# Performance work log

Measured on AMD Instinct MI355X. Metric: run time of the kernel, lower is better.

The kernel has to match this reference:

```python
import jax, jax.numpy as jnp
import numpy as np

B, T, C, H = 8, 2048, 1024, 128

def setup_inputs() -> dict:
    key = jax.random.key(0)
    kx, kq, kk, kv = jax.random.split(key, 4)
    x = jax.random.normal(kx, (B, T, C), dtype=jnp.float32)
    Wq = jax.random.normal(kq, (C, H), dtype=jnp.float32) * 0.02
    Wk = jax.random.normal(kk, (C, H), dtype=jnp.float32) * 0.02
    Wv = jax.random.normal(kv, (C, H), dtype=jnp.float32) * 0.02
    return {"x": x, "Wq": Wq, "Wk": Wk, "Wv": Wv}

def reference(x, Wq, Wk, Wv):
    # q,k,v: [B,T,H] via bias-free dense projections
    q = jnp.einsum('btc,ch->bth', x, Wq)
    k = jnp.einsum('btc,ch->bth', x, Wk)
    v = jnp.einsum('btc,ch->bth', x, Wv)
    scale = k.shape[-1] ** (-0.5)
    # scores: [B,T,T]
    wei = jnp.einsum('bth,bsh->bts', q, k) * scale
    Tlen = x.shape[1]
    causal = jnp.tril(jnp.ones((Tlen, Tlen), dtype=bool))  # True = keep
    wei = jnp.where(causal[None, :, :], wei, -jnp.inf)
    wei = jax.nn.softmax(wei, axis=-1)
    return jnp.einsum('bts,bsh->bth', wei, v)
```

## Files before the change

kernel.cpp:

```cpp
#include <hip/hip_runtime.h>

#define B_ 8
#define T_ 2048
#define C_ 1024
#define H_ 128
#define BT_ (B_*T_)

typedef unsigned short u16;
typedef unsigned int u32;
typedef __attribute__((ext_vector_type(4))) float f32x4;
typedef __attribute__((ext_vector_type(8))) __bf16 bf16x8;

__device__ __forceinline__ u16 f2bf(float f) {
  u32 u = __float_as_uint(f);
  u += 0x7fffu + ((u >> 16) & 1u);
  return (u16)(u >> 16);
}

#define GLL16(g, l) __builtin_amdgcn_global_load_lds( \
    (const __attribute__((address_space(1))) void*)(g), \
    (__attribute__((address_space(3))) void*)(l), 16, 0, 0)

__device__ __forceinline__ bf16x8 load_frag(const u16* base, int stride, int row0, int k0, int lane) {
  const u16* p = base + (size_t)(row0 + (lane & 15)) * stride + k0 + ((lane >> 4) << 3);
  return *reinterpret_cast<const bf16x8*>(p);
}

__device__ __forceinline__ bf16x8 cvt8(f32x4 lo, f32x4 hi) {
  union { u16 h[8]; bf16x8 v; } u;
#pragma unroll
  for (int i = 0; i < 4; i++) { u.h[i] = f2bf(lo[i]); u.h[4 + i] = f2bf(hi[i]); }
  return u.v;
}

__global__ void wt_kernel(const float* __restrict__ Wq, const float* __restrict__ Wk,
                          const float* __restrict__ Wv, u16* __restrict__ wt) {
  int mat = blockIdx.y;
  const float* W = (mat == 0) ? Wq : (mat == 1) ? Wk : Wv;
  int i = blockIdx.x * 256 + threadIdx.x;
  int h = i >> 10;
  int c = i & 1023;
  wt[mat * (C_ * H_) + i] = f2bf(W[c * H_ + h]);
}

__global__ __launch_bounds__(256) void qkv_gemm(const float* __restrict__ x, const u16* __restrict__ wt,
                                                u16* __restrict__ q, u16* __restrict__ k2,
                                                u16* __restrict__ vt) {
  __shared__ __align__(16) float As[2][64 * 32];
  __shared__ __align__(16) u16 Bs[2][128 * 32];
  int t = threadIdx.x;
  int lane = t & 63, w = t >> 6;
  int wm = w >> 1, wn = w & 1;
  int quad = lane >> 4, col = lane & 15;
  int m0 = blockIdx.x * 64;
  int mat = blockIdx.y;
  const u16* wmp = wt + (size_t)mat * (C_ * H_);

  int ar0 = t >> 3, ar1 = ar0 + 32;
  const float* ax0 = x + (size_t)(m0 + ar0) * C_ + (((t & 7) ^ (ar0 & 7)) << 2);
  const float* ax1 = x + (size_t)(m0 + ar1) * C_ + (((t & 7) ^ (ar1 & 7)) << 2);
  const u16* bw0 = wmp + (size_t)(t >> 2) * C_ + ((t & 3) << 3);
  const u16* bw1 = bw0 + (size_t)64 * C_;

  GLL16(ax0, &As[0][w * 256]);
  GLL16(ax1, &As[0][w * 256 + 1024]);
  GLL16(bw0, &Bs[0][w * 512]);
  GLL16(bw1, &Bs[0][2048 + w * 512]);

  f32x4 acc[2][4] = {};
  for (int kk = 0; kk < 32; kk++) {
    int cur = kk & 1;
    __syncthreads();
    if (kk + 1 < 32) {
      int nxt = cur ^ 1;
      int kn = (kk + 1) * 32;
      GLL16(ax0 + kn, &As[nxt][w * 256]);
      GLL16(ax1 + kn, &As[nxt][w * 256 + 1024]);
      GLL16(bw0 + kn, &Bs[nxt][w * 512]);
      GLL16(bw1 + kn, &Bs[nxt][2048 + w * 512]);
    }
    const float* Ab = &As[cur][0];
    const u16* Bb = &Bs[cur][0];
    bf16x8 af[2];
#pragma unroll
    for (int mt = 0; mt < 2; mt++) {
      int r = wm * 32 + mt * 16 + col;
      int s0 = (quad * 2) ^ (r & 7);
      int s1 = s0 ^ 1;
      f32x4 lo = *reinterpret_cast<const f32x4*>(Ab + r * 32 + s0 * 4);
      f32x4 hi = *reinterpret_cast<const f32x4*>(Ab + r * 32 + s1 * 4);
      af[mt] = cvt8(lo, hi);
    }
    bf16x8 bfr[4];
#pragma unroll
    for (int nt = 0; nt < 4; nt++) {
      int n = wn * 64 + nt * 16 + col;
      bfr[nt] = *reinterpret_cast<const bf16x8*>(Bb + n * 32 + quad * 8);
    }
#pragma unroll
    for (int mt = 0; mt < 2; mt++)
#pragma unroll
      for (int nt = 0; nt < 4; nt++)
        acc[mt][nt] = __builtin_amdgcn_mfma_f32_16x16x32_bf16(af[mt], bfr[nt], acc[mt][nt], 0, 0, 0);
  }

#pragma unroll
  for (int mt = 0; mt < 2; mt++) {
    int row0 = m0 + wm * 32 + mt * 16 + quad * 4;
#pragma unroll
    for (int nt = 0; nt < 4; nt++) {
      int n = wn * 64 + nt * 16 + col;
      if (mat == 0) {
#pragma unroll
        for (int r = 0; r < 4; r++) q[(size_t)(row0 + r) * H_ + n] = f2bf(acc[mt][nt][r]);
      } else if (mat == 1) {
#pragma unroll
        for (int r = 0; r < 4; r++) k2[(size_t)(row0 + r) * H_ + n] = f2bf(acc[mt][nt][r]);
      } else {
        int bb = row0 >> 11, tt = row0 & 2047;
        ushort4 pk;
        pk.x = f2bf(acc[mt][nt][0]); pk.y = f2bf(acc[mt][nt][1]);
        pk.z = f2bf(acc[mt][nt][2]); pk.w = f2bf(acc[mt][nt][3]);
        *reinterpret_cast<ushort4*>(&vt[((size_t)bb * H_ + n) * T_ + tt]) = pk;
      }
    }
  }
}

__global__ __launch_bounds__(256) void attn_part(const u16* __restrict__ q, const u16* __restrict__ k,
                                                 const u16* __restrict__ vt,
                                                 float* __restrict__ Op, float* __restrict__ lsum) {
  __shared__ __align__(16) u16 Ks[2][32 * 136];
  __shared__ __align__(16) u16 Vs[2][128 * 40];
  __shared__ __align__(16) u16 P[4][2][16 * 40];
  int t = threadIdx.x;
  int lane = t & 63, w = t >> 6;
  int quad = lane >> 4, col = lane & 15;
  int bx = blockIdx.x;
  int qt = 31 - (bx >> 4);
  int s = (bx >> 3) & 1;
  int b = bx & 7;
  const float scale = 0.08838834764831845f;

  int nk = 2 * (qt + 1);
  int n0 = qt + 1;
  int it0 = s ? n0 : 0;
  int it1 = s ? nk : n0;

  int krow0 = t >> 4, ke = (t & 15) * 8;
  int krow1 = krow0 + 16;
  int vrow0 = t >> 2, ve = (t & 3) * 8;
  int vrow1 = vrow0 + 64;

  int qrow0 = b * T_ + qt * 64 + w * 16;
  bf16x8 qf[4];
#pragma unroll
  for (int ks = 0; ks < 4; ks++) qf[ks] = load_frag(q, H_, qrow0, ks * 32, lane);

  f32x4 o[8] = {};
  float l[4] = {0.f, 0.f, 0.f, 0.f};
  int myqrow = qt * 64 + w * 16 + quad * 4;

  {
    const u16* kb = k + (size_t)(b * T_ + it0 * 32) * H_;
    *reinterpret_cast<uint4*>(&Ks[0][krow0 * 136 + ke]) = *reinterpret_cast<const uint4*>(kb + (size_t)krow0 * 128 + ke);
    *reinterpret_cast<uint4*>(&Ks[0][krow1 * 136 + ke]) = *reinterpret_cast<const uint4*>(kb + (size_t)krow1 * 128 + ke);
    const u16* vb = vt + (size_t)b * H_ * T_ + it0 * 32;
    *reinterpret_cast<uint4*>(&Vs[0][vrow0 * 40 + ve]) = *reinterpret_cast<const uint4*>(vb + (size_t)vrow0 * T_ + ve);
    *reinterpret_cast<uint4*>(&Vs[0][vrow1 * 40 + ve]) = *reinterpret_cast<const uint4*>(vb + (size_t)vrow1 * T_ + ve);
  }

  for (int kt = it0; kt < it1; kt++) {
    int cur = (kt - it0) & 1;
    __syncthreads();
    bool more = (kt + 1 < it1);
    uint4 kc0, kc1, vc0, vc1;
    if (more) {
      const u16* kb = k + (size_t)(b * T_ + (kt + 1) * 32) * H_;
      kc0 = *reinterpret_cast<const uint4*>(kb + (size_t)krow0 * 128 + ke);
      kc1 = *reinterpret_cast<const uint4*>(kb + (size_t)krow1 * 128 + ke);
      const u16* vb = vt + (size_t)b * H_ * T_ + (kt + 1) * 32;
      vc0 = *reinterpret_cast<const uint4*>(vb + (size_t)vrow0 * T_ + ve);
      vc1 = *reinterpret_cast<const uint4*>(vb + (size_t)vrow1 * T_ + ve);
    }

    f32x4 s0 = {}, s1 = {};
#pragma unroll
    for (int ks = 0; ks < 4; ks++) {
      bf16x8 kb0 = *reinterpret_cast<const bf16x8*>(&Ks[cur][col * 136 + ks * 32 + quad * 8]);
      bf16x8 kb1 = *reinterpret_cast<const bf16x8*>(&Ks[cur][(col + 16) * 136 + ks * 32 + quad * 8]);
      s0 = __builtin_amdgcn_mfma_f32_16x16x32_bf16(qf[ks], kb0, s0, 0, 0, 0);
      s1 = __builtin_amdgcn_mfma_f32_16x16x32_bf16(qf[ks], kb1, s1, 0, 0, 0);
    }

    float pv[8];
    int kcol0 = kt * 32 + col;
#pragma unroll
    for (int r = 0; r < 4; r++) {
      int qr = myqrow + r;
      float a0 = fminf(s0[r] * scale, 30.f);
      float a1 = fminf(s1[r] * scale, 30.f);
      a0 = (kcol0      > qr) ? -1e30f : a0;
      a1 = (kcol0 + 16 > qr) ? -1e30f : a1;
      float p0 = __expf(a0);
      float p1 = __expf(a1);
      pv[r] = p0; pv[4 + r] = p1;
      l[r] += p0 + p1;
    }

    u16* Pb = &P[w][cur][0];
#pragma unroll
    for (int r = 0; r < 4; r++) {
      Pb[(quad * 4 + r) * 40 + col] = f2bf(pv[r]);
      Pb[(quad * 4 + r) * 40 + col + 16] = f2bf(pv[4 + r]);
    }
    asm volatile("" ::: "memory");
    __builtin_amdgcn_s_waitcnt(0xc07f);
    asm volatile("" ::: "memory");
    bf16x8 pf = *reinterpret_cast<const bf16x8*>(&Pb[col * 40 + (quad << 3)]);

#pragma unroll
    for (int ht = 0; ht < 8; ht++) {
      bf16x8 vf = *reinterpret_cast<const bf16x8*>(&Vs[cur][(ht * 16 + col) * 40 + quad * 8]);
      o[ht] = __builtin_amdgcn_mfma_f32_16x16x32_bf16(pf, vf, o[ht], 0, 0, 0);
    }

    if (more) {
      int nxt = cur ^ 1;
      *reinterpret_cast<uint4*>(&Ks[nxt][krow0 * 136 + ke]) = kc0;
      *reinterpret_cast<uint4*>(&Ks[nxt][krow1 * 136 + ke]) = kc1;
      *reinterpret_cast<uint4*>(&Vs[nxt][vrow0 * 40 + ve]) = vc0;
      *reinterpret_cast<uint4*>(&Vs[nxt][vrow1 * 40 + ve]) = vc1;
    }
  }

#pragma unroll
  for (int r = 0; r < 4; r++) {
    float v = l[r];
    v += __shfl_xor(v, 1);
    v += __shfl_xor(v, 2);
    v += __shfl_xor(v, 4);
    v += __shfl_xor(v, 8);
    l[r] = v;
  }

  int tile = (s * 8 + b) * 32 + qt;
  float* Orow = Op + (size_t)tile * (64 * 128);
  float* lrow = lsum + (size_t)tile * 64;
  int rowin0 = w * 16 + quad * 4;
  if (col == 0) {
#pragma unroll
    for (int r = 0; r < 4; r++) lrow[rowin0 + r] = l[r];
  }
#pragma unroll
  for (int ht = 0; ht < 8; ht++) {
#pragma unroll
    for (int r = 0; r < 4; r++)
      Orow[(size_t)(rowin0 + r) * 128 + ht * 16 + col] = o[ht][r];
  }
}

__global__ __launch_bounds__(256) void attn_comb(const float* __restrict__ Op, const float* __restrict__ lsum,
                                                 float* __restrict__ out) {
  int bx = blockIdx.x;
  int b = bx >> 5, qt = bx & 31;
  int t = threadIdx.x;
  int h = t & 127, half = t >> 7;
  int tile0 = b * 32 + qt;
  int tile1 = tile0 + 256;
#pragma unroll 4
  for (int rr = 0; rr < 32; rr++) {
    int row = half * 32 + rr;
    float l0 = lsum[tile0 * 64 + row];
    float l1 = lsum[tile1 * 64 + row];
    float rl = 1.f / (l0 + l1);
    float v = (Op[(size_t)tile0 * 8192 + row * 128 + h] +
               Op[(size_t)tile1 * 8192 + row * 128 + h]) * rl;
    out[((size_t)(b * T_ + qt * 64 + row)) * H_ + h] = v;
  }
}

extern "C" void kernel_launch(void* const* d_in, const int* in_sizes, int n_in,
                              void* d_out, int out_size, void* d_ws, size_t ws_size,
                              hipStream_t stream) {
  (void)in_sizes; (void)n_in; (void)out_size; (void)ws_size;
  const float* x  = (const float*)d_in[0];
  const float* Wq = (const float*)d_in[1];
  const float* Wk = (const float*)d_in[2];
  const float* Wv = (const float*)d_in[3];
  u16* ws = (u16*)d_ws;
  u16* q  = ws;
  u16* k  = ws + (size_t)BT_ * H_;
  u16* vt = ws + 2 * (size_t)BT_ * H_;
  u16* wt = ws + 3 * (size_t)BT_ * H_;
  float* Op = (float*)(ws + 3 * (size_t)BT_ * H_ + 3 * C_ * H_);
  float* lsum = Op + (size_t)512 * 64 * 128;
  float* out = (float*)d_out;

  wt_kernel<<<dim3(512, 3), 256, 0, stream>>>(Wq, Wk, Wv, wt);
  qkv_gemm<<<dim3(BT_ / 64, 3), 256, 0, stream>>>(x, wt, q, k, vt);
  attn_part<<<dim3(512), 256, 0, stream>>>(q, k, vt, Op, lsum);
  attn_comb<<<dim3(256), 256, 0, stream>>>(Op, lsum, out);
}
```

Baseline: 175.6 us.

## Deepen QKV GEMM pipeline to 4-stage LDS ring with explicit vmcnt waits

Replaces the double-buffered K loop in the QKV projection GEMM with a 4-buffer LDS ring that keeps three stages of global-to-LDS loads in flight. Each iteration waits with an explicit s_waitcnt vmcnt(8) and a raw barrier, then issues the stage three iterations ahead. The aim is to hide more global-load latency. It also swaps the manual round-to-nearest bf16 conversion for native __bf16 casts, which may lower to hardware convert instructions. The ring doubles LDS use and may reduce occupancy. The trailing iterations issue redundant wrapped loads (stage index mod 32). Correctness relies on the hand-written vmcnt count matching the number of outstanding loads.

```diff
diff --git a/kernel.cpp b/kernel.cpp
--- a/kernel.cpp
+++ b/kernel.cpp
@@ -26,11 +26,11 @@
   return *reinterpret_cast<const bf16x8*>(p);
 }
 
-__device__ __forceinline__ bf16x8 cvt8(f32x4 lo, f32x4 hi) {
-  union { u16 h[8]; bf16x8 v; } u;
-#pragma unroll
-  for (int i = 0; i < 4; i++) { u.h[i] = f2bf(lo[i]); u.h[4 + i] = f2bf(hi[i]); }
-  return u.v;
+__device__ __forceinline__ bf16x8 cvt8n(f32x4 lo, f32x4 hi) {
+  bf16x8 r;
+#pragma unroll
+  for (int i = 0; i < 4; i++) { r[i] = (__bf16)lo[i]; r[4 + i] = (__bf16)hi[i]; }
+  return r;
 }
 
 __global__ void wt_kernel(const float* __restrict__ Wq, const float* __restrict__ Wk,
@@ -46,8 +46,8 @@
 __global__ __launch_bounds__(256) void qkv_gemm(const float* __restrict__ x, const u16* __restrict__ wt,
                                                 u16* __restrict__ q, u16* __restrict__ k2,
                                                 u16* __restrict__ vt) {
-  __shared__ __align__(16) float As[2][64 * 32];
-  __shared__ __align__(16) u16 Bs[2][128 * 32];
+  __shared__ __align__(16) float As[4][64 * 32];
+  __shared__ __align__(16) u16 Bs[4][128 * 32];
   int t = threadIdx.x;
   int lane = t & 63, w = t >> 6;
   int wm = w >> 1, wn = w & 1;
@@ -62,25 +62,30 @@
   const u16* bw0 = wmp + (size_t)(t >> 2) * C_ + ((t & 3) << 3);
   const u16* bw1 = bw0 + (size_t)64 * C_;
 
-  GLL16(ax0, &As[0][w * 256]);
-  GLL16(ax1, &As[0][w * 256 + 1024]);
-  GLL16(bw0, &Bs[0][w * 512]);
-  GLL16(bw1, &Bs[0][2048 + w * 512]);
+#define STAGE(st, buf) do { \
+    int ko_ = (st) * 32; \
+    GLL16(ax0 + ko_, &As[buf][w * 256]); \
+    GLL16(ax1 + ko_, &As[buf][w * 256 + 1024]); \
+    GLL16(bw0 + ko_, &Bs[buf][w * 512]); \
+    GLL16(bw1 + ko_, &Bs[buf][2048 + w * 512]); \
+  } while (0)
+
+  STAGE(0, 0);
+  STAGE(1, 1);
+  STAGE(2, 2);
 
   f32x4 acc[2][4] = {};
+#pragma unroll 4
   for (int kk = 0; kk < 32; kk++) {
-    int cur = kk & 1;
-    __syncthreads();
-    if (kk + 1 < 32) {
-      int nxt = cur ^ 1;
-      int kn = (kk + 1) * 32;
-      GLL16(ax0 + kn, &As[nxt][w * 256]);
-      GLL16(ax1 + kn, &As[nxt][w * 256 + 1024]);
-      GLL16(bw0 + kn, &Bs[nxt][w * 512]);
-      GLL16(bw1 + kn, &Bs[nxt][2048 + w * 512]);
-    }
-    const float* Ab = &As[cur][0];
-    const u16* Bb = &Bs[cur][0];
+    asm volatile("s_waitcnt vmcnt(8)" ::: "memory");
+    __builtin_amdgcn_s_barrier();
+    asm volatile("" ::: "memory");
+    {
+      int st = (kk + 3) & 31;
+      STAGE(st, (kk + 3) & 3);
+    }
+    const float* Ab = &As[kk & 3][0];
+    const u16* Bb = &Bs[kk & 3][0];
     bf16x8 af[2];
 #pragma unroll
     for (int mt = 0; mt < 2; mt++) {
@@ -89,7 +94,7 @@
       int s1 = s0 ^ 1;
       f32x4 lo = *reinterpret_cast<const f32x4*>(Ab + r * 32 + s0 * 4);
       f32x4 hi = *reinterpret_cast<const f32x4*>(Ab + r * 32 + s1 * 4);
-      af[mt] = cvt8(lo, hi);
+      af[mt] = cvt8n(lo, hi);
     }
     bf16x8 bfr[4];
 #pragma unroll
@@ -103,6 +108,7 @@
       for (int nt = 0; nt < 4; nt++)
         acc[mt][nt] = __builtin_amdgcn_mfma_f32_16x16x32_bf16(af[mt], bfr[nt], acc[mt][nt], 0, 0, 0);
   }
+#undef STAGE
 
 #pragma unroll
   for (int mt = 0; mt < 2; mt++) {
```

New measurement: 174.9 us. Within noise of the previous version (-0.4%).
